# Optimization experiments

Hardware: AMD Instinct MI355X
Metric: run time of the kernel (lower is better)

The kernel has to match this reference:

```python
import jax, jax.numpy as jnp
import numpy as np

LAMBDA_N = 0.01
OUTER_LOOP = 2
INNER_LOOP = 50
MAX_DIST = 0.1
LR = 0.2
LR_DECAY = 0.1
ADAGRAD_EPS = 1e-10


def _normalize(x, eps=1e-12):
    # torch F.normalize: x / max(||x||, eps)
    n = jnp.linalg.norm(x, axis=-1, keepdims=True)
    return x / jnp.maximum(n, eps)


def _interp_bary(tri, vw):
    # tri: [b, n, 3, 3] (3 corners x 3 coords), vw: [b, n, 2]
    bary = jnp.concatenate([vw, 1.0 - vw[..., :1] - vw[..., 1:2]], axis=-1)  # [b,n,3]
    return jnp.einsum('bnij,bni->bnj', tri, bary)


def setup_inputs() -> dict:
    key = jax.random.key(0)
    k0, k1, k2, k3, k4 = jax.random.split(key, 5)
    B, Np, Nv, Nf = 1, 8192, 16384, 16384
    query_V = jax.random.uniform(k0, (B, Np, 3), dtype=jnp.float32)
    query_N = _normalize(jax.random.normal(k1, (B, Np, 3), dtype=jnp.float32))
    mesh_V = jax.random.uniform(k2, (Nv, 3), dtype=jnp.float32)
    mesh_F = jax.random.randint(k3, (Nf, 3), 0, Nv, dtype=jnp.int64)
    mesh_N = _normalize(jax.random.normal(k4, (Nv, 3), dtype=jnp.float32))
    return {'query_V': query_V, 'query_N': query_N, 'mesh_V': mesh_V,
            'mesh_F': mesh_F, 'mesh_N': mesh_N}


def reference(query_V, query_N, mesh_V, mesh_F, mesh_N):
    # ---- init_corres_spt: brute-force KNN (K=1) to face centers ----
    F_centers = mesh_V[mesh_F].mean(axis=1)                     # [Nf, 3]
    # squared distances [B, Np, Nf] (pytorch3d knn_points returns squared dist)
    d2 = (jnp.sum(query_V * query_V, axis=-1, keepdims=True)
          - 2.0 * jnp.einsum('bnd,fd->bnf', query_V, F_centers)
          + jnp.sum(F_centers * F_centers, axis=-1))
    spt_fidx = jnp.argmin(d2, axis=-1)                          # [B, Np]
    dmin = jnp.min(d2, axis=-1)
    outlier_mask = dmin > MAX_DIST
    valid = ~outlier_mask
    mask = valid.astype(query_V.dtype)                          # [B, Np]
    denom = jnp.maximum(jnp.sum(mask), 1.0)

    spt_vw0 = jnp.full(query_V.shape[:-1] + (2,), 1.0 / 3.0, dtype=query_V.dtype)

    tri = mesh_F[spt_fidx]          # [B, Np, 3] vertex indices (gather)
    tri_V = mesh_V[tri]             # [B, Np, 3, 3]
    tri_N = mesh_N[tri]             # [B, Np, 3, 3]

    def loss_fn(delta, vw_base):
        vw = vw_base + delta
        corres_V = _interp_bary(tri_V, vw)
        loss_v = jnp.linalg.norm(corres_V - query_V, axis=-1)   # [B, Np]
        corres_N = _normalize(_interp_bary(tri_N, vw))
        loss_n = jnp.linalg.norm(corres_N - query_N, axis=-1)
        per_point = loss_v + LAMBDA_N * loss_n
        # masked mean over valid points only (original indexes out valid points)
        return jnp.sum(per_point * mask) / denom

    grad_fn = jax.grad(loss_fn)

    def solve_delta_vw(vw_base):
        # Adagrad(lr=0.2, lr_decay=0.1), 50 steps
        def step(carry, i):
            delta, ssum = carry
            g = grad_fn(delta, vw_base)
            ssum = ssum + g * g
            clr = LR / (1.0 + i * LR_DECAY)
            delta = delta - clr * g / (jnp.sqrt(ssum) + ADAGRAD_EPS)
            return (delta, ssum), None
        z = jnp.zeros_like(vw_base)
        (delta, _), _ = jax.lax.scan(step, (z, z),
                                     jnp.arange(INNER_LOOP, dtype=vw_base.dtype))
        return delta

    # ---- update_corres_spt: outer loop with alpha halving ----
    vw = spt_vw0
    alpha = 1.0
    for _ in range(OUTER_LOOP):
        delta = solve_delta_vw(vw)
        vw = vw + delta * alpha       # triwalk fallback: spt_vw + spt_delta
        alpha = alpha * 0.5

    # invalid (outlier) points keep their init barycentric coords
    spt_vw = jnp.where(valid[..., None], vw, spt_vw0)
    return spt_fidx, spt_vw, outlier_mask
```

## Files before the change

### kernel.cpp

```cpp
#include <hip/hip_runtime.h>
#include <math.h>

#define NP 8192
#define NF 16384
#define GQ 8
#define MARGIN 1e-5f

__global__ __launch_bounds__(256) void k_centers(const float* __restrict__ mV,
                                                 const int* __restrict__ mF,
                                                 double* __restrict__ ctr,
                                                 float4* __restrict__ ctrf,
                                                 double* __restrict__ clrtab) {
    if (blockIdx.x == 0 && threadIdx.x < 50) {
        clrtab[threadIdx.x] = 0.2 / (1.0 + (double)threadIdx.x * 0.1);
    }
    int f = blockIdx.x * 256 + threadIdx.x;
    if (f >= NF) return;
    int i0 = mF[3*f+0], i1 = mF[3*f+1], i2 = mF[3*f+2];
    double cx = ((double)mV[3*i0+0] + (double)mV[3*i1+0] + (double)mV[3*i2+0]) / 3.0;
    double cy = ((double)mV[3*i0+1] + (double)mV[3*i1+1] + (double)mV[3*i2+1]) / 3.0;
    double cz = ((double)mV[3*i0+2] + (double)mV[3*i1+2] + (double)mV[3*i2+2]) / 3.0;
    double cc = cx*cx + cy*cy + cz*cz;
    ctr[4*f+0] = cx; ctr[4*f+1] = cy; ctr[4*f+2] = cz; ctr[4*f+3] = cc;
    ctrf[f] = make_float4((float)cx, (float)cy, (float)cz, (float)cc);
}

__global__ __launch_bounds__(256) void k_knn(const float* __restrict__ qV,
                                             const float4* __restrict__ ctrf,
                                             const double* __restrict__ ctr,
                                             float* __restrict__ out,
                                             int* __restrict__ fidx_ws,
                                             int* __restrict__ valid_ws,
                                             int* __restrict__ flag) {
    int pbase = blockIdx.x * GQ;
    float qx[GQ], qy[GQ], qz[GQ];
    #pragma unroll
    for (int g = 0; g < GQ; ++g) {
        int p = pbase + g;
        qx[g] = qV[3*p+0];
        qy[g] = qV[3*p+1];
        qz[g] = qV[3*p+2];
    }
    float b1[GQ], b2[GQ]; int i1[GQ];
    #pragma unroll
    for (int g = 0; g < GQ; ++g) { b1[g] = 1e30f; b2[g] = 1e30f; i1[g] = 0x7fffffff; }

    #pragma unroll 2
    for (int f = threadIdx.x; f < NF; f += 256) {
        float4 c = ctrf[f];
        #pragma unroll
        for (int g = 0; g < GQ; ++g) {
            float dot = qx[g]*c.x + qy[g]*c.y + qz[g]*c.z;
            float key = c.w - 2.0f*dot;
            float ob1 = b1[g];
            bool lt = key < ob1;
            b1[g] = lt ? key : ob1;
            i1[g] = lt ? f : i1[g];
            float cand2 = lt ? ob1 : key;
            b2[g] = cand2 < b2[g] ? cand2 : b2[g];
        }
    }
    #pragma unroll
    for (int off = 32; off > 0; off >>= 1) {
        #pragma unroll
        for (int g = 0; g < GQ; ++g) {
            float ob1 = __shfl_down(b1[g], off);
            int   oi1 = __shfl_down(i1[g], off);
            float ob2 = __shfl_down(b2[g], off);
            bool win = (ob1 < b1[g]) || (ob1 == b1[g] && oi1 < i1[g]);
            float loser = win ? b1[g] : ob1;
            b1[g] = win ? ob1 : b1[g];
            i1[g] = win ? oi1 : i1[g];
            float mb2 = ob2 < b2[g] ? ob2 : b2[g];
            b2[g] = loser < mb2 ? loser : mb2;
        }
    }
    __shared__ float sv1[4][GQ], sv2[4][GQ];
    __shared__ int   si1[4][GQ];
    int wid = threadIdx.x >> 6, lane = threadIdx.x & 63;
    if (lane == 0) {
        #pragma unroll
        for (int g = 0; g < GQ; ++g) { sv1[wid][g] = b1[g]; si1[wid][g] = i1[g]; sv2[wid][g] = b2[g]; }
    }
    __syncthreads();
    if (threadIdx.x == 0) {
        const double4* ctr4 = (const double4*)ctr;
        for (int g = 0; g < GQ; ++g) {
            float bv = sv1[0][g], r2 = sv2[0][g]; int bi = si1[0][g];
            for (int w2 = 1; w2 < 4; ++w2) {
                float ob1 = sv1[w2][g], ob2 = sv2[w2][g]; int oi1 = si1[w2][g];
                bool win = (ob1 < bv) || (ob1 == bv && oi1 < bi);
                float loser = win ? bv : ob1;
                bv = win ? ob1 : bv;
                bi = win ? oi1 : bi;
                float mb2 = ob2 < r2 ? ob2 : r2;
                r2 = loser < mb2 ? loser : mb2;
            }
            int p = pbase + g;
            flag[p] = (r2 - bv < MARGIN) ? 1 : 0;
            double4 c = ctr4[bi];
            double dqx = (double)qx[g], dqy = (double)qy[g], dqz = (double)qz[g];
            double dot = dqx*c.x + dqy*c.y + dqz*c.z;
            double qq  = dqx*dqx + dqy*dqy + dqz*dqz;
            double d2  = (qq - 2.0*dot) + c.w;
            int outlier = (d2 > 0.1) ? 1 : 0;
            fidx_ws[p]  = bi;
            valid_ws[p] = 1 - outlier;
            out[p]        = (float)bi;
            out[3*NP + p] = outlier ? 1.0f : 0.0f;
        }
    }
}

__global__ __launch_bounds__(256) void k_repair(const float* __restrict__ qV,
                                                const double* __restrict__ ctr,
                                                const int* __restrict__ flag,
                                                float* __restrict__ out,
                                                int* __restrict__ fidx_ws,
                                                int* __restrict__ valid_ws) {
    int p = blockIdx.x;
    if (!flag[p]) return;
    double qx = (double)qV[3*p+0], qy = (double)qV[3*p+1], qz = (double)qV[3*p+2];
    double best = 1e300; int bidx = 0x7fffffff;
    const double4* ctr4 = (const double4*)ctr;
    for (int f = threadIdx.x; f < NF; f += 256) {
        double4 c = ctr4[f];
        double dot = qx*c.x + qy*c.y + qz*c.z;
        double key = c.w - 2.0*dot;
        if (key < best) { best = key; bidx = f; }
    }
    #pragma unroll
    for (int off = 32; off > 0; off >>= 1) {
        double ov = __shfl_down(best, off);
        int    oi = __shfl_down(bidx, off);
        if (ov < best || (ov == best && oi < bidx)) { best = ov; bidx = oi; }
    }
    __shared__ double sv[4];
    __shared__ int    si[4];
    int wid = threadIdx.x >> 6, lane = threadIdx.x & 63;
    if (lane == 0) { sv[wid] = best; si[wid] = bidx; }
    __syncthreads();
    if (threadIdx.x == 0) {
        double bv = sv[0]; int bi = si[0];
        for (int w2 = 1; w2 < 4; ++w2) {
            double ov = sv[w2]; int oi = si[w2];
            if (ov < bv || (ov == bv && oi < bi)) { bv = ov; bi = oi; }
        }
        double4 c = ctr4[bi];
        double dot = qx*c.x + qy*c.y + qz*c.z;
        double qq  = qx*qx + qy*qy + qz*qz;
        double d2  = (qq - 2.0*dot) + c.w;
        int outlier = (d2 > 0.1) ? 1 : 0;
        fidx_ws[p]  = bi;
        valid_ws[p] = 1 - outlier;
        out[p]        = (float)bi;
        out[3*NP + p] = outlier ? 1.0f : 0.0f;
    }
}

__global__ __launch_bounds__(256) void k_denom(const int* __restrict__ valid_ws,
                                               double* __restrict__ denom) {
    __shared__ int s[256];
    int acc = 0;
    for (int i = threadIdx.x; i < NP; i += 256) acc += valid_ws[i];
    s[threadIdx.x] = acc;
    __syncthreads();
    for (int off = 128; off > 0; off >>= 1) {
        if (threadIdx.x < off) s[threadIdx.x] += s[threadIdx.x + off];
        __syncthreads();
    }
    if (threadIdx.x == 0) {
        double d = (double)s[0];
        denom[0] = d > 1.0 ? d : 1.0;
    }
}

__global__ __launch_bounds__(256) void k_opt(const float* __restrict__ qV,
                                             const float* __restrict__ qN,
                                             const float* __restrict__ mV,
                                             const int* __restrict__ mF,
                                             const float* __restrict__ mN,
                                             const int* __restrict__ fidx_ws,
                                             const int* __restrict__ valid_ws,
                                             const double* __restrict__ denomp,
                                             const double* __restrict__ clrtab,
                                             float* __restrict__ out) {
    int p = blockIdx.x * 256 + threadIdx.x;
    if (p >= NP) return;
    const float third = (float)(1.0/3.0);
    if (!valid_ws[p]) {
        out[NP + 2*p + 0] = third;
        out[NP + 2*p + 1] = third;
        return;
    }
    double inv_denom = 1.0 / denomp[0];
    int f = fidx_ws[p];
    int i0 = mF[3*f+0], i1 = mF[3*f+1], i2 = mF[3*f+2];

    double V0x = mV[3*i0+0], V0y = mV[3*i0+1], V0z = mV[3*i0+2];
    double V1x = mV[3*i1+0], V1y = mV[3*i1+1], V1z = mV[3*i1+2];
    double V2x = mV[3*i2+0], V2y = mV[3*i2+1], V2z = mV[3*i2+2];
    double N0x = mN[3*i0+0], N0y = mN[3*i0+1], N0z = mN[3*i0+2];
    double N1x = mN[3*i1+0], N1y = mN[3*i1+1], N1z = mN[3*i1+2];
    double N2x = mN[3*i2+0], N2y = mN[3*i2+1], N2z = mN[3*i2+2];
    double qx  = qV[3*p+0],  qy  = qV[3*p+1],  qz  = qV[3*p+2];
    double qnx = qN[3*p+0],  qny = qN[3*p+1],  qnz = qN[3*p+2];

    double Eux = V0x - V2x, Euy = V0y - V2y, Euz = V0z - V2z;
    double Ewx = V1x - V2x, Ewy = V1y - V2y, Ewz = V1z - V2z;
    double Fux = N0x - N2x, Fuy = N0y - N2y, Fuz = N0z - N2z;
    double Fwx = N1x - N2x, Fwy = N1y - N2y, Fwz = N1z - N2z;
    double Kx  = V2x - qx,  Ky  = V2y - qy,  Kz  = V2z - qz;

    double u = 1.0/3.0, w = 1.0/3.0;
    double alpha = 1.0;
    for (int outer = 0; outer < 2; ++outer) {
        double du = 0.0, dw = 0.0, su = 0.0, sw = 0.0;
        for (int it = 0; it < 50; ++it) {
            double uu = u + du, ww = w + dw;
            double rvx = uu*Eux + ww*Ewx + Kx;
            double rvy = uu*Euy + ww*Ewy + Ky;
            double rvz = uu*Euz + ww*Ewz + Kz;
            double L2v = rvx*rvx + rvy*rvy + rvz*rvz;
            double invLv = rsqrt(L2v);
            double gu = (rvx*Eux + rvy*Euy + rvz*Euz) * invLv;
            double gw = (rvx*Ewx + rvy*Ewy + rvz*Ewz) * invLv;
            double nx = uu*Fux + ww*Fwx + N2x;
            double ny = uu*Fuy + ww*Fwy + N2y;
            double nz = uu*Fuz + ww*Fwz + N2z;
            double m2 = nx*nx + ny*ny + nz*nz;
            bool   mok = (m2 > 1e-24);
            double inv = mok ? rsqrt(m2) : 1e12;
            double hx = nx*inv, hy = ny*inv, hz = nz*inv;
            double rnx = hx - qnx, rny = hy - qny, rnz = hz - qnz;
            double L2n = rnx*rnx + rny*rny + rnz*rnz;
            double invLn = rsqrt(L2n);
            double A_u = rnx*Fux + rny*Fuy + rnz*Fuz;
            double A_w = rnx*Fwx + rny*Fwy + rnz*Fwz;
            double B   = rnx*nx + rny*ny + rnz*nz;
            double C_u = nx*Fux + ny*Fuy + nz*Fuz;
            double C_w = nx*Fwx + ny*Fwy + nz*Fwz;
            double s = mok ? ((B*inv)*inv)*inv : 0.0;
            double gnu = (A_u*inv - s*C_u) * invLn;
            double gnw = (A_w*inv - s*C_w) * invLn;
            gu = (gu + 0.01*gnu) * inv_denom;
            gw = (gw + 0.01*gnw) * inv_denom;
            su += gu*gu; sw += gw*gw;
            double clr = clrtab[it];
            du -= clr * gu / (sqrt(su) + 1e-10);
            dw -= clr * gw / (sqrt(sw) + 1e-10);
        }
        u += du * alpha; w += dw * alpha;
        alpha *= 0.5;
    }
    out[NP + 2*p + 0] = (float)u;
    out[NP + 2*p + 1] = (float)w;
}

extern "C" void kernel_launch(void* const* d_in, const int* in_sizes, int n_in,
                              void* d_out, int out_size, void* d_ws, size_t ws_size,
                              hipStream_t stream) {
    const float* qV = (const float*)d_in[0];
    const float* qN = (const float*)d_in[1];
    const float* mV = (const float*)d_in[2];
    const int*   mF = (const int*)d_in[3];
    const float* mN = (const float*)d_in[4];
    float* out = (float*)d_out;

    double* ctr      = (double*)d_ws;
    double* denom    = ctr + (size_t)NF*4;
    double* clrtab   = denom + 1;
    float4* ctrf     = (float4*)(clrtab + 50);
    int*    flag     = (int*)(ctrf + NF);
    int*    fidx_ws  = flag + NP;
    int*    valid_ws = fidx_ws + NP;

    hipLaunchKernelGGL(k_centers, dim3(NF/256), dim3(256), 0, stream, mV, mF, ctr, ctrf, clrtab);
    hipLaunchKernelGGL(k_knn,     dim3(NP/GQ),  dim3(256), 0, stream, qV, ctrf, ctr,
                       out, fidx_ws, valid_ws, flag);
    hipLaunchKernelGGL(k_repair,  dim3(NP),     dim3(256), 0, stream, qV, ctr, flag,
                       out, fidx_ws, valid_ws);
    hipLaunchKernelGGL(k_denom,   dim3(1),      dim3(256), 0, stream, valid_ws, denom);
    hipLaunchKernelGGL(k_opt,     dim3(NP/256), dim3(256), 0, stream,
                       qV, qN, mV, mF, mN, fidx_ws, valid_ws, denom, clrtab, out);
}
```

Baseline: 121.8 us.

## Fuse double-precision KNN repair into the KNN kernel and halve queries per block

Moves the fp64 re-scan for near-tie queries out of a separate repair kernel and into the KNN kernel, so flagged queries are re-checked in place. This drops the repair launch, which spawned one block per query, and the flag array round-trip. GQ drops from 8 to 4, doubling the block count, and the inner min/second-min update now uses fminf/fmaxf. The fused fp64 loop adds block-wide syncs inside the KNN kernel, and fewer queries per block means each center load is reused by fewer queries.

```diff
diff --git a/kernel.cpp b/kernel.cpp
--- a/kernel.cpp
+++ b/kernel.cpp
@@ -3,7 +3,7 @@
 
 #define NP 8192
 #define NF 16384
-#define GQ 8
+#define GQ 4
 #define MARGIN 1e-5f
 
 __global__ __launch_bounds__(256) void k_centers(const float* __restrict__ mV,
@@ -30,16 +30,13 @@
                                              const double* __restrict__ ctr,
                                              float* __restrict__ out,
                                              int* __restrict__ fidx_ws,
-                                             int* __restrict__ valid_ws,
-                                             int* __restrict__ flag) {
+                                             int* __restrict__ valid_ws) {
     int pbase = blockIdx.x * GQ;
     float qx[GQ], qy[GQ], qz[GQ];
     #pragma unroll
     for (int g = 0; g < GQ; ++g) {
         int p = pbase + g;
-        qx[g] = qV[3*p+0];
-        qy[g] = qV[3*p+1];
-        qz[g] = qV[3*p+2];
+        qx[g] = qV[3*p+0]; qy[g] = qV[3*p+1]; qz[g] = qV[3*p+2];
     }
     float b1[GQ], b2[GQ]; int i1[GQ];
     #pragma unroll
@@ -52,12 +49,11 @@
         for (int g = 0; g < GQ; ++g) {
             float dot = qx[g]*c.x + qy[g]*c.y + qz[g]*c.z;
             float key = c.w - 2.0f*dot;
-            float ob1 = b1[g];
-            bool lt = key < ob1;
-            b1[g] = lt ? key : ob1;
+            bool  lt  = key < b1[g];
+            float cand2 = fmaxf(key, b1[g]);
+            b2[g] = fminf(b2[g], cand2);
             i1[g] = lt ? f : i1[g];
-            float cand2 = lt ? ob1 : key;
-            b2[g] = cand2 < b2[g] ? cand2 : b2[g];
+            b1[g] = lt ? key : b1[g];
         }
     }
     #pragma unroll
@@ -71,12 +67,13 @@
             float loser = win ? b1[g] : ob1;
             b1[g] = win ? ob1 : b1[g];
             i1[g] = win ? oi1 : i1[g];
-            float mb2 = ob2 < b2[g] ? ob2 : b2[g];
-            b2[g] = loser < mb2 ? loser : mb2;
+            b2[g] = fminf(loser, fminf(ob2, b2[g]));
         }
     }
     __shared__ float sv1[4][GQ], sv2[4][GQ];
     __shared__ int   si1[4][GQ];
+    __shared__ int   rbi[GQ];
+    __shared__ int   rfl[GQ];
     int wid = threadIdx.x >> 6, lane = threadIdx.x & 63;
     if (lane == 0) {
         #pragma unroll
@@ -84,7 +81,6 @@
     }
     __syncthreads();
     if (threadIdx.x == 0) {
-        const double4* ctr4 = (const double4*)ctr;
         for (int g = 0; g < GQ; ++g) {
             float bv = sv1[0][g], r2 = sv2[0][g]; int bi = si1[0][g];
             for (int w2 = 1; w2 < 4; ++w2) {
@@ -93,13 +89,53 @@
                 float loser = win ? bv : ob1;
                 bv = win ? ob1 : bv;
                 bi = win ? oi1 : bi;
-                float mb2 = ob2 < r2 ? ob2 : r2;
-                r2 = loser < mb2 ? loser : mb2;
+                r2 = fminf(loser, fminf(ob2, r2));
             }
+            rbi[g] = bi;
+            rfl[g] = (r2 - bv < MARGIN) ? 1 : 0;
+        }
+    }
+    __syncthreads();
+
+    const double4* ctr4 = (const double4*)ctr;
+    __shared__ double dsv[4];
+    __shared__ int    dsi[4];
+    for (int g = 0; g < GQ; ++g) {
+        if (!rfl[g]) continue;
+        int p = pbase + g;
+        double dqx = (double)qV[3*p+0], dqy = (double)qV[3*p+1], dqz = (double)qV[3*p+2];
+        double best = 1e300; int bidx = 0x7fffffff;
+        for (int f = threadIdx.x; f < NF; f += 256) {
+            double4 c = ctr4[f];
+            double dot = dqx*c.x + dqy*c.y + dqz*c.z;
+            double key = c.w - 2.0*dot;
+            if (key < best) { best = key; bidx = f; }
+        }
+        #pragma unroll
+        for (int off = 32; off > 0; off >>= 1) {
+            double ov = __shfl_down(best, off);
+            int    oi = __shfl_down(bidx, off);
+            if (ov < best || (ov == best && oi < bidx)) { best = ov; bidx = oi; }
+        }
+        if (lane == 0) { dsv[wid] = best; dsi[wid] = bidx; }
+        __syncthreads();
+        if (threadIdx.x == 0) {
+            double bv = dsv[0]; int bi = dsi[0];
+            for (int w2 = 1; w2 < 4; ++w2) {
+                double ov = dsv[w2]; int oi = dsi[w2];
+                if (ov < bv || (ov == bv && oi < bi)) { bv = ov; bi = oi; }
+            }
+            rbi[g] = bi;
+        }
+        __syncthreads();
+    }
+
+    if (threadIdx.x == 0) {
+        for (int g = 0; g < GQ; ++g) {
             int p = pbase + g;
-            flag[p] = (r2 - bv < MARGIN) ? 1 : 0;
+            int bi = rbi[g];
             double4 c = ctr4[bi];
-            double dqx = (double)qx[g], dqy = (double)qy[g], dqz = (double)qz[g];
+            double dqx = (double)qV[3*p+0], dqy = (double)qV[3*p+1], dqz = (double)qV[3*p+2];
             double dot = dqx*c.x + dqy*c.y + dqz*c.z;
             double qq  = dqx*dqx + dqy*dqy + dqz*dqz;
             double d2  = (qq - 2.0*dot) + c.w;
@@ -109,52 +145,6 @@
             out[p]        = (float)bi;
             out[3*NP + p] = outlier ? 1.0f : 0.0f;
         }
-    }
-}
-
-__global__ __launch_bounds__(256) void k_repair(const float* __restrict__ qV,
-                                                const double* __restrict__ ctr,
-                                                const int* __restrict__ flag,
-                                                float* __restrict__ out,
-                                                int* __restrict__ fidx_ws,
-                                                int* __restrict__ valid_ws) {
-    int p = blockIdx.x;
-    if (!flag[p]) return;
-    double qx = (double)qV[3*p+0], qy = (double)qV[3*p+1], qz = (double)qV[3*p+2];
-    double best = 1e300; int bidx = 0x7fffffff;
-    const double4* ctr4 = (const double4*)ctr;
-    for (int f = threadIdx.x; f < NF; f += 256) {
-        double4 c = ctr4[f];
-        double dot = qx*c.x + qy*c.y + qz*c.z;
-        double key = c.w - 2.0*dot;
-        if (key < best) { best = key; bidx = f; }
-    }
-    #pragma unroll
-    for (int off = 32; off > 0; off >>= 1) {
-        double ov = __shfl_down(best, off);
-        int    oi = __shfl_down(bidx, off);
-        if (ov < best || (ov == best && oi < bidx)) { best = ov; bidx = oi; }
-    }
-    __shared__ double sv[4];
-    __shared__ int    si[4];
-    int wid = threadIdx.x >> 6, lane = threadIdx.x & 63;
-    if (lane == 0) { sv[wid] = best; si[wid] = bidx; }
-    __syncthreads();
-    if (threadIdx.x == 0) {
-        double bv = sv[0]; int bi = si[0];
-        for (int w2 = 1; w2 < 4; ++w2) {
-            double ov = sv[w2]; int oi = si[w2];
-            if (ov < bv || (ov == bv && oi < bi)) { bv = ov; bi = oi; }
-        }
-        double4 c = ctr4[bi];
-        double dot = qx*c.x + qy*c.y + qz*c.z;
-        double qq  = qx*qx + qy*qy + qz*qz;
-        double d2  = (qq - 2.0*dot) + c.w;
-        int outlier = (d2 > 0.1) ? 1 : 0;
-        fidx_ws[p]  = bi;
-        valid_ws[p] = 1 - outlier;
-        out[p]        = (float)bi;
-        out[3*NP + p] = outlier ? 1.0f : 0.0f;
     }
 }
 
@@ -271,15 +261,13 @@
     double* denom    = ctr + (size_t)NF*4;
     double* clrtab   = denom + 1;
     float4* ctrf     = (float4*)(clrtab + 50);
-    int*    flag     = (int*)(ctrf + NF);
-    int*    fidx_ws  = flag + NP;
+    int*    fidx_ws  = (int*)(ctrf + NF);
     int*    valid_ws = fidx_ws + NP;
 
-    hipLaunchKernelGGL(k_centers, dim3(NF/256), dim3(256), 0, stream, mV, mF, ctr, ctrf, clrtab);
-    hipLaunchKernelGGL(k_knn,     dim3(NP/GQ),  dim3(256), 0, stream, qV, ctrf, ctr,
-                       out, fidx_ws, valid_ws, flag);
-    hipLaunchKernelGGL(k_repair,  dim3(NP),     dim3(256), 0, stream, qV, ctr, flag,
-                       out, fidx_ws, valid_ws);
+    hipLaunchKernelGGL(k_centers, dim3(NF/256), dim3(256), 0, stream,
+                       mV, mF, ctr, ctrf, clrtab);
+    hipLaunchKernelGGL(k_knn,     dim3(NP/GQ),  dim3(256), 0, stream,
+                       qV, ctrf, ctr, out, fidx_ws, valid_ws);
     hipLaunchKernelGGL(k_denom,   dim3(1),      dim3(256), 0, stream, valid_ws, denom);
     hipLaunchKernelGGL(k_opt,     dim3(NP/256), dim3(256), 0, stream,
                        qV, qN, mV, mF, mN, fidx_ws, valid_ws, denom, clrtab, out);
```

Result: faster. 116.6 us (-4.2%).
